# Kernel tuning notes

Hardware: AMD Instinct MI355X
Metric: run time of the kernel (lower is better)

Reference implementation:

```python
import jax, jax.numpy as jnp
import numpy as np
import math

B, S, C, H = 1, 4096, 512, 8
BLOCK = 64
NUM_RANDOM = 3


def _bigbird_mask(key):
    idx = jnp.arange(S)
    # window attention: |i - j| <= block_size // 2
    win = jnp.abs(idx[:, None] - idx[None, :]) <= (BLOCK // 2)
    # random attention: NUM_RANDOM random columns per row
    cols = jax.random.randint(key, (S, NUM_RANDOM), 0, S)
    rnd = jnp.zeros((S, S), dtype=bool).at[idx[:, None], cols].set(True)
    mask = win | rnd
    # global attention: first/last row and column attend/are attended everywhere
    mask = mask.at[0, :].set(True).at[-1, :].set(True)
    mask = mask.at[:, 0].set(True).at[:, -1].set(True)
    return mask


def setup_inputs() -> dict:
    key = jax.random.key(0)
    ks = jax.random.split(key, 7)
    xavier = lambda k: jax.random.uniform(k, (C, C), jnp.float32, -1.0, 1.0) * math.sqrt(6.0 / (C + C))
    return {
        "x": jax.random.normal(ks[0], (B, S, C), jnp.float32),
        "attn_mask": _bigbird_mask(ks[1]),
        "Wq": xavier(ks[2]), "bq": jnp.zeros((C,), jnp.float32),
        "Wk": xavier(ks[3]), "bk": jnp.zeros((C,), jnp.float32),
        "Wv": xavier(ks[4]), "bv": jnp.zeros((C,), jnp.float32),
        "Wo": xavier(ks[5]), "bo": jnp.zeros((C,), jnp.float32),
    }


def reference(x, attn_mask, Wq, bq, Wk, bk, Wv, bv, Wo, bo):
    b, s, c = x.shape
    dh = c // H
    # projections (torch Linear: x @ W.T + b)
    q = (x @ Wq.T + bq).reshape(b, s, H, dh).transpose(0, 2, 1, 3)  # [B,H,S,Dh]
    k = (x @ Wk.T + bk).reshape(b, s, H, dh).transpose(0, 2, 1, 3)
    v = (x @ Wv.T + bv).reshape(b, s, H, dh).transpose(0, 2, 1, 3)
    scores = jnp.einsum("bhsd,bhtd->bhst", q, k) / math.sqrt(dh)  # [B,H,S,S]
    scores = jnp.where(attn_mask[None, None], scores, -jnp.inf)
    attn = jax.nn.softmax(scores, axis=-1)
    out = jnp.einsum("bhst,bhtd->bhsd", attn, v)
    out = out.transpose(0, 2, 1, 3).reshape(b, s, c)
    return out @ Wo.T + bo
```

## Files before the change

### kernel.cpp

```cpp
#include <hip/hip_runtime.h>
#include <hip/hip_bf16.h>
#include <cstdint>
#include <cstddef>

#define S_LEN 4096
#define C_DIM 512
#define H_NUM 8
#define DH 64
#define MAXC 80
#define NSPLIT 64
#define DENSE_TASKS 16

typedef short short8 __attribute__((ext_vector_type(8)));
typedef float f32x4 __attribute__((ext_vector_type(4)));

__device__ __forceinline__ unsigned short f2bf(float f) {
  union { float f; uint32_t u; } c; c.f = f;
  uint32_t u = c.u;
  uint32_t r = (u + 0x7fffu + ((u >> 16) & 1u)) >> 16;
  return (unsigned short)r;
}
__device__ __forceinline__ float bf2f(unsigned short h) {
  union { uint32_t u; float f; } c; c.u = ((uint32_t)h) << 16;
  return c.f;
}

__global__ __launch_bounds__(256) void split_bf16(const float* __restrict__ src,
                                                  unsigned short* __restrict__ hi,
                                                  unsigned short* __restrict__ lo,
                                                  int n4) {
  int idx = blockIdx.x * 256 + threadIdx.x;
  if (idx >= n4) return;
  float4 v = ((const float4*)src)[idx];
  ushort4 h, l;
  h.x = f2bf(v.x); l.x = f2bf(v.x - bf2f(h.x));
  h.y = f2bf(v.y); l.y = f2bf(v.y - bf2f(h.y));
  h.z = f2bf(v.z); l.z = f2bf(v.z - bf2f(h.z));
  h.w = f2bf(v.w); l.w = f2bf(v.w - bf2f(h.w));
  ((ushort4*)hi)[idx] = h;
  ((ushort4*)lo)[idx] = l;
}

__device__ __forceinline__ void gemm_mfma_body(
    const unsigned short* __restrict__ Ah, const unsigned short* __restrict__ Al,
    const unsigned short* __restrict__ Bh, const unsigned short* __restrict__ Bl,
    const float* __restrict__ bias, float* __restrict__ C) {
  const int lane = threadIdx.x & 63;
  const int wave = threadIdx.x >> 6;
  const int m_base = blockIdx.y * 128 + (wave >> 1) * 64;
  const int n_base = blockIdx.x * 64 + (wave & 1) * 32;
  const int rfrag = lane & 15;
  const int koff = (lane >> 4) * 8;

  f32x4 acc[4][2];
#pragma unroll
  for (int mi = 0; mi < 4; ++mi)
#pragma unroll
    for (int ni = 0; ni < 2; ++ni) acc[mi][ni] = (f32x4){0.f, 0.f, 0.f, 0.f};

  for (int ks = 0; ks < C_DIM; ks += 32) {
    const int kb = ks + koff;
    short8 ah[4], al[4], bh[2], bl[2];
#pragma unroll
    for (int mi = 0; mi < 4; ++mi) {
      const size_t off = (size_t)(m_base + mi * 16 + rfrag) * C_DIM + kb;
      ah[mi] = *(const short8*)(Ah + off);
      al[mi] = *(const short8*)(Al + off);
    }
#pragma unroll
    for (int ni = 0; ni < 2; ++ni) {
      const size_t off = (size_t)(n_base + ni * 16 + rfrag) * C_DIM + kb;
      bh[ni] = *(const short8*)(Bh + off);
      bl[ni] = *(const short8*)(Bl + off);
    }
#pragma unroll
    for (int mi = 0; mi < 4; ++mi)
#pragma unroll
      for (int ni = 0; ni < 2; ++ni) {
        acc[mi][ni] = __builtin_amdgcn_mfma_f32_16x16x32_bf16(ah[mi], bh[ni], acc[mi][ni], 0, 0, 0);
        acc[mi][ni] = __builtin_amdgcn_mfma_f32_16x16x32_bf16(ah[mi], bl[ni], acc[mi][ni], 0, 0, 0);
        acc[mi][ni] = __builtin_amdgcn_mfma_f32_16x16x32_bf16(al[mi], bh[ni], acc[mi][ni], 0, 0, 0);
      }
  }

  const int col = lane & 15;
  const int r0 = (lane >> 4) * 4;
#pragma unroll
  for (int mi = 0; mi < 4; ++mi)
#pragma unroll
    for (int ni = 0; ni < 2; ++ni) {
      const float b = bias[n_base + ni * 16 + col];
#pragma unroll
      for (int r = 0; r < 4; ++r) {
        C[(size_t)(m_base + mi * 16 + r0 + r) * C_DIM + n_base + ni * 16 + col] =
            acc[mi][ni][r] + b;
      }
    }
}

__global__ __launch_bounds__(256) void qkv_gemm_mfma(
    const unsigned short* __restrict__ xh, const unsigned short* __restrict__ xl,
    const unsigned short* __restrict__ W4h, const unsigned short* __restrict__ W4l,
    const float* __restrict__ bq, const float* __restrict__ bk,
    const float* __restrict__ bv, float* __restrict__ Qbase) {
  const int z = blockIdx.z;
  const size_t NW = (size_t)C_DIM * C_DIM;
  const float* bias = (z == 0) ? bq : (z == 1) ? bk : bv;
  gemm_mfma_body(xh, xl, W4h + z * NW, W4l + z * NW, bias,
                 Qbase + z * (size_t)S_LEN * C_DIM);
}

__global__ __launch_bounds__(256) void o_gemm_mfma(
    const unsigned short* __restrict__ AOh, const unsigned short* __restrict__ AOl,
    const unsigned short* __restrict__ W4h, const unsigned short* __restrict__ W4l,
    const float* __restrict__ bo, float* __restrict__ out) {
  const size_t NW = (size_t)C_DIM * C_DIM;
  gemm_mfma_body(AOh, AOl, W4h + 3 * NW, W4l + 3 * NW, bo, out);
}

__global__ __launch_bounds__(256) void scan_mask(const uint32_t* __restrict__ mask32,
                                                 int* __restrict__ counts,
                                                 int* __restrict__ cols) {
  int i = blockIdx.x;
  int tid = threadIdx.x;
  if (i == 0 || i == S_LEN - 1) {
    if (tid == 0) counts[i] = 0;
    return;
  }
  __shared__ int cnt;
  __shared__ int list[MAXC];
  if (tid == 0) cnt = 0;
  __syncthreads();

  const bool is_b32 = (mask32[0] == 1u);
  if (is_b32) {
    const uint4* m4 = (const uint4*)(mask32 + (size_t)i * S_LEN);
#pragma unroll
    for (int q = 0; q < 4; ++q) {
      uint4 v = m4[tid * 4 + q];
      int base = tid * 16 + q * 4;
      if (v.x) { int p = atomicAdd(&cnt, 1); if (p < MAXC) list[p] = base + 0; }
      if (v.y) { int p = atomicAdd(&cnt, 1); if (p < MAXC) list[p] = base + 1; }
      if (v.z) { int p = atomicAdd(&cnt, 1); if (p < MAXC) list[p] = base + 2; }
      if (v.w) { int p = atomicAdd(&cnt, 1); if (p < MAXC) list[p] = base + 3; }
    }
  } else {
    const uint8_t* mrow = (const uint8_t*)mask32 + (size_t)i * S_LEN;
    uint4 mv = ((const uint4*)mrow)[tid];
    uint32_t w[4] = {mv.x, mv.y, mv.z, mv.w};
#pragma unroll
    for (int q = 0; q < 4; ++q)
#pragma unroll
      for (int b = 0; b < 4; ++b) {
        if ((w[q] >> (8 * b)) & 0xffu) {
          int p = atomicAdd(&cnt, 1);
          if (p < MAXC) list[p] = tid * 16 + q * 4 + b;
        }
      }
  }
  __syncthreads();
  int n = cnt < MAXC ? cnt : MAXC;
  if (tid == 0) counts[i] = n;
  for (int t = tid; t < n; t += 256) cols[(size_t)i * MAXC + t] = list[t];
}

__global__ __launch_bounds__(256) void attn_sparse(
    const float* __restrict__ Q, const float* __restrict__ K,
    const float* __restrict__ V, const int* __restrict__ counts,
    const int* __restrict__ cols, float* __restrict__ AO) {
  int wid = threadIdx.x >> 6, lane = threadIdx.x & 63;
  int task = blockIdx.x * 4 + wid;
  int i = task >> 3, h = task & 7;
  if (i == 0 || i == S_LEN - 1) return;

  __shared__ float q_lds[4][DH];
  __shared__ float ps[4][MAXC];
  __shared__ int   cs[4][MAXC];

  q_lds[wid][lane] = Q[(size_t)i * C_DIM + h * DH + lane];
  asm volatile("s_waitcnt lgkmcnt(0)" ::: "memory");
  const float4* q4 = (const float4*)q_lds[wid];

  int n = counts[i];
  if (n < 1) {
    AO[(size_t)i * C_DIM + h * DH + lane] = 0.f;
    return;
  }
  const int* cl = cols + (size_t)i * MAXC;
  int c0 = (lane < n) ? cl[lane] : 0;
  int c1 = (64 + lane < n) ? cl[64 + lane] : -1;
  bool act0 = lane < n;

  float s0 = -INFINITY, s1 = -INFINITY;
  if (act0) {
    const float4* kp = (const float4*)(K + (size_t)c0 * C_DIM + h * DH);
    float s = 0.f;
#pragma unroll
    for (int dd = 0; dd < 16; ++dd) {
      float4 kv = kp[dd], qv = q4[dd];
      s += qv.x * kv.x + qv.y * kv.y + qv.z * kv.z + qv.w * kv.w;
    }
    s0 = s * 0.125f;
  }
  if (c1 >= 0) {
    const float4* kp = (const float4*)(K + (size_t)c1 * C_DIM + h * DH);
    float s = 0.f;
#pragma unroll
    for (int dd = 0; dd < 16; ++dd) {
      float4 kv = kp[dd], qv = q4[dd];
      s += qv.x * kv.x + qv.y * kv.y + qv.z * kv.z + qv.w * kv.w;
    }
    s1 = s * 0.125f;
  }

  float mx = fmaxf(s0, s1);
#pragma unroll
  for (int off = 32; off; off >>= 1) mx = fmaxf(mx, __shfl_xor(mx, off));
  float p0 = __expf(s0 - mx);
  float p1 = __expf(s1 - mx);
  float l = p0 + p1;
#pragma unroll
  for (int off = 32; off; off >>= 1) l += __shfl_xor(l, off);
  float rl = 1.0f / l;

  ps[wid][lane] = p0 * rl;
  cs[wid][lane] = c0;
  if (lane < MAXC - 64) {
    ps[wid][64 + lane] = (c1 >= 0) ? p1 * rl : 0.f;
    cs[wid][64 + lane] = (c1 >= 0) ? c1 : 0;
  }
  asm volatile("s_waitcnt lgkmcnt(0)" ::: "memory");

  float acc = 0.f;
  const float* Vh = V + h * DH + lane;
  const int npad = (n + 7) & ~7;
  for (int j0 = 0; j0 < npad; j0 += 8) {
    float pj[8], vv[8];
#pragma unroll
    for (int u = 0; u < 8; ++u) {
      int cj = cs[wid][j0 + u];
      pj[u] = ps[wid][j0 + u];
      vv[u] = Vh[(size_t)cj * C_DIM];
    }
#pragma unroll
    for (int u = 0; u < 8; ++u) acc = fmaf(pj[u], vv[u], acc);
  }
  AO[(size_t)i * C_DIM + h * DH + lane] = acc;
}

__global__ __launch_bounds__(256) void attn_dense(const float* __restrict__ Q,
                                                  const float* __restrict__ K,
                                                  const float* __restrict__ V,
                                                  float* __restrict__ part) {
  int wid = threadIdx.x >> 6, lane = threadIdx.x & 63;
  int gid = blockIdx.x * 4 + wid;
  int task = gid >> 6;
  int split = gid & 63;
  int i = (task >> 3) ? (S_LEN - 1) : 0;
  int h = task & 7;

  __shared__ float q_lds[4][DH];
  __shared__ float pd[4][64];
  q_lds[wid][lane] = Q[(size_t)i * C_DIM + h * DH + lane];
  asm volatile("s_waitcnt lgkmcnt(0)" ::: "memory");
  const float4* q4 = (const float4*)q_lds[wid];

  const int c = split * 64 + lane;
  const float4* kp = (const float4*)(K + (size_t)c * C_DIM + h * DH);
  float s = 0.f;
#pragma unroll
  for (int dd = 0; dd < 16; ++dd) {
    float4 kv = kp[dd], qv = q4[dd];
    s += qv.x * kv.x + qv.y * kv.y + qv.z * kv.z + qv.w * kv.w;
  }
  s *= 0.125f;
  float m = s;
#pragma unroll
  for (int off = 32; off; off >>= 1) m = fmaxf(m, __shfl_xor(m, off));
  float p = __expf(s - m);
  float l = p;
#pragma unroll
  for (int off = 32; off; off >>= 1) l += __shfl_xor(l, off);

  pd[wid][lane] = p;
  asm volatile("s_waitcnt lgkmcnt(0)" ::: "memory");

  float acc = 0.f;
  const float* Vb = V + (size_t)(split * 64) * C_DIM + h * DH + lane;
  for (int j0 = 0; j0 < 64; j0 += 8) {
    float pj[8], vv[8];
#pragma unroll
    for (int u = 0; u < 8; ++u) {
      pj[u] = pd[wid][j0 + u];
      vv[u] = Vb[(size_t)(j0 + u) * C_DIM];
    }
#pragma unroll
    for (int u = 0; u < 8; ++u) acc = fmaf(pj[u], vv[u], acc);
  }
  float* pt = part + (size_t)(task * NSPLIT + split) * 68;
  pt[lane] = acc;
  if (lane == 0) {
    pt[64] = m;
    pt[65] = l;
  }
}

__global__ __launch_bounds__(64) void attn_combine(const float* __restrict__ part,
                                                   float* __restrict__ AO) {
  int task = blockIdx.x;
  int lane = threadIdx.x;
  float m = -INFINITY;
  for (int sp = 0; sp < NSPLIT; ++sp)
    m = fmaxf(m, part[(size_t)(task * NSPLIT + sp) * 68 + 64]);
  float l = 0.f, acc = 0.f;
  for (int sp = 0; sp < NSPLIT; ++sp) {
    const float* pt = part + (size_t)(task * NSPLIT + sp) * 68;
    float w = __expf(pt[64] - m);
    l += w * pt[65];
    acc += w * pt[lane];
  }
  int i = (task >> 3) ? (S_LEN - 1) : 0;
  int h = task & 7;
  AO[(size_t)i * C_DIM + h * DH + lane] = acc / l;
}

extern "C" void kernel_launch(void* const* d_in, const int* in_sizes, int n_in,
                              void* d_out, int out_size, void* d_ws,
                              size_t ws_size, hipStream_t stream) {
  const float* x = (const float*)d_in[0];
  const uint32_t* mask = (const uint32_t*)d_in[1];
  const float* Wq = (const float*)d_in[2];
  const float* bq = (const float*)d_in[3];
  const float* Wk = (const float*)d_in[4];
  const float* bk = (const float*)d_in[5];
  const float* Wv = (const float*)d_in[6];
  const float* bv = (const float*)d_in[7];
  const float* Wo = (const float*)d_in[8];
  const float* bo = (const float*)d_in[9];
  float* out = (float*)d_out;

  const size_t NELT = (size_t)S_LEN * C_DIM;
  const size_t NW = (size_t)C_DIM * C_DIM;

  float* Q = (float*)d_ws;
  float* Kb = Q + NELT;
  float* Vb = Kb + NELT;
  float* AO = Vb + NELT;
  int* counts = (int*)(AO + NELT);
  int* colsl = counts + S_LEN;
  float* part = (float*)(colsl + (size_t)S_LEN * MAXC);
  unsigned short* xh = (unsigned short*)(part + (size_t)DENSE_TASKS * NSPLIT * 68);
  unsigned short* xl = xh + NELT;
  unsigned short* AOh = xl + NELT;
  unsigned short* AOl = AOh + NELT;
  unsigned short* W4h = AOl + NELT;
  unsigned short* W4l = W4h + 4 * NW;

  scan_mask<<<S_LEN, 256, 0, stream>>>(mask, counts, colsl);

  split_bf16<<<(NELT / 4 + 255) / 256, 256, 0, stream>>>(x, xh, xl, NELT / 4);
  split_bf16<<<(NW / 4 + 255) / 256, 256, 0, stream>>>(Wq, W4h, W4l, NW / 4);
  split_bf16<<<(NW / 4 + 255) / 256, 256, 0, stream>>>(Wk, W4h + NW, W4l + NW, NW / 4);
  split_bf16<<<(NW / 4 + 255) / 256, 256, 0, stream>>>(Wv, W4h + 2 * NW, W4l + 2 * NW, NW / 4);
  split_bf16<<<(NW / 4 + 255) / 256, 256, 0, stream>>>(Wo, W4h + 3 * NW, W4l + 3 * NW, NW / 4);
  qkv_gemm_mfma<<<dim3(C_DIM / 64, S_LEN / 128, 3), 256, 0, stream>>>(
      xh, xl, W4h, W4l, bq, bk, bv, Q);

  attn_sparse<<<(S_LEN * H_NUM) / 4, 256, 0, stream>>>(Q, Kb, Vb, counts, colsl, AO);
  attn_dense<<<(DENSE_TASKS * NSPLIT) / 4, 256, 0, stream>>>(Q, Kb, Vb, part);
  attn_combine<<<DENSE_TASKS, 64, 0, stream>>>(part, AO);

  split_bf16<<<(NELT / 4 + 255) / 256, 256, 0, stream>>>(AO, AOh, AOl, NELT / 4);
  o_gemm_mfma<<<dim3(C_DIM / 64, S_LEN / 128, 1), 256, 0, stream>>>(
      AOh, AOl, W4h, W4l, bo, out);
}
```

Measured before the change: 354.8 us.

## Cooperative K-row loads in sparse attention, merge weight splits, swizzle block order

The sparse attention score step now has 16 lanes handle one column each, with 4 lanes splitting each K row into 16-float slices and reducing with shuffles. Scores go through LDS instead of each lane reading a whole 64-float K row on its own. This is meant to give coalesced K reads and avoid idle lanes when a row has fewer than 64 valid columns. Block indices are swizzled across the grid and launch bounds raised to aim for more occupancy, and the four weight-split launches become one 2D launch to save launch overhead. It adds a serial chunk loop, extra LDS traffic, and shuffle reductions.

```diff
diff --git a/kernel.cpp b/kernel.cpp
--- a/kernel.cpp
+++ b/kernel.cpp
@@ -23,6 +23,13 @@
 __device__ __forceinline__ float bf2f(unsigned short h) {
   union { uint32_t u; float f; } c; c.u = ((uint32_t)h) << 16;
   return c.f;
+}
+
+__device__ __forceinline__ void split4(float4 v, ushort4& h, ushort4& l) {
+  h.x = f2bf(v.x); l.x = f2bf(v.x - bf2f(h.x));
+  h.y = f2bf(v.y); l.y = f2bf(v.y - bf2f(h.y));
+  h.z = f2bf(v.z); l.z = f2bf(v.z - bf2f(h.z));
+  h.w = f2bf(v.w); l.w = f2bf(v.w - bf2f(h.w));
 }
 
 __global__ __launch_bounds__(256) void split_bf16(const float* __restrict__ src,
@@ -33,12 +40,24 @@
   if (idx >= n4) return;
   float4 v = ((const float4*)src)[idx];
   ushort4 h, l;
-  h.x = f2bf(v.x); l.x = f2bf(v.x - bf2f(h.x));
-  h.y = f2bf(v.y); l.y = f2bf(v.y - bf2f(h.y));
-  h.z = f2bf(v.z); l.z = f2bf(v.z - bf2f(h.z));
-  h.w = f2bf(v.w); l.w = f2bf(v.w - bf2f(h.w));
+  split4(v, h, l);
   ((ushort4*)hi)[idx] = h;
   ((ushort4*)lo)[idx] = l;
+}
+
+__global__ __launch_bounds__(256) void split_bf16_w4(
+    const float* __restrict__ Wq, const float* __restrict__ Wk,
+    const float* __restrict__ Wv, const float* __restrict__ Wo,
+    unsigned short* __restrict__ W4h, unsigned short* __restrict__ W4l) {
+  const int z = blockIdx.y;
+  const float* src = (z == 0) ? Wq : (z == 1) ? Wk : (z == 2) ? Wv : Wo;
+  const size_t NW4 = (size_t)C_DIM * C_DIM / 4;
+  int idx = blockIdx.x * 256 + threadIdx.x;
+  float4 v = ((const float4*)src)[idx];
+  ushort4 h, l;
+  split4(v, h, l);
+  ((ushort4*)(W4h))[z * NW4 + idx] = h;
+  ((ushort4*)(W4l))[z * NW4 + idx] = l;
 }
 
 __device__ __forceinline__ void gemm_mfma_body(
@@ -164,55 +183,57 @@
   for (int t = tid; t < n; t += 256) cols[(size_t)i * MAXC + t] = list[t];
 }
 
-__global__ __launch_bounds__(256) void attn_sparse(
+__global__ __launch_bounds__(256, 8) void attn_sparse(
     const float* __restrict__ Q, const float* __restrict__ K,
     const float* __restrict__ V, const int* __restrict__ counts,
     const int* __restrict__ cols, float* __restrict__ AO) {
+  int bid = blockIdx.x;
+  int bid2 = (bid & 7) * (int)(gridDim.x >> 3) + (bid >> 3);
   int wid = threadIdx.x >> 6, lane = threadIdx.x & 63;
-  int task = blockIdx.x * 4 + wid;
+  int task = bid2 * 4 + wid;
   int i = task >> 3, h = task & 7;
   if (i == 0 || i == S_LEN - 1) return;
 
   __shared__ float q_lds[4][DH];
+  __shared__ float sc[4][MAXC];
   __shared__ float ps[4][MAXC];
   __shared__ int   cs[4][MAXC];
 
+  int n = counts[i];
   q_lds[wid][lane] = Q[(size_t)i * C_DIM + h * DH + lane];
-  asm volatile("s_waitcnt lgkmcnt(0)" ::: "memory");
-  const float4* q4 = (const float4*)q_lds[wid];
-
-  int n = counts[i];
+  const int* cl = cols + (size_t)i * MAXC;
+  cs[wid][lane] = (lane < n) ? cl[lane] : 0;
+  if (lane < MAXC - 64) cs[wid][64 + lane] = (64 + lane < n) ? cl[64 + lane] : 0;
+  asm volatile("s_waitcnt lgkmcnt(0)" ::: "memory");
+
   if (n < 1) {
     AO[(size_t)i * C_DIM + h * DH + lane] = 0.f;
     return;
   }
-  const int* cl = cols + (size_t)i * MAXC;
-  int c0 = (lane < n) ? cl[lane] : 0;
-  int c1 = (64 + lane < n) ? cl[64 + lane] : -1;
-  bool act0 = lane < n;
-
-  float s0 = -INFINITY, s1 = -INFINITY;
-  if (act0) {
-    const float4* kp = (const float4*)(K + (size_t)c0 * C_DIM + h * DH);
+
+  const int qq = lane >> 4, c = lane & 15;
+  const float* qrow = q_lds[wid] + qq * 16;
+  const int nchunk = (n + 15) >> 4;
+  for (int ch = 0; ch < nchunk; ++ch) {
+    int col = cs[wid][ch * 16 + c];
+    const float4* kp = (const float4*)(K + (size_t)col * C_DIM + h * DH + qq * 16);
+    float4 kr[4];
+#pragma unroll
+    for (int dd = 0; dd < 4; ++dd) kr[dd] = kp[dd];
     float s = 0.f;
 #pragma unroll
-    for (int dd = 0; dd < 16; ++dd) {
-      float4 kv = kp[dd], qv = q4[dd];
-      s += qv.x * kv.x + qv.y * kv.y + qv.z * kv.z + qv.w * kv.w;
-    }
-    s0 = s * 0.125f;
-  }
-  if (c1 >= 0) {
-    const float4* kp = (const float4*)(K + (size_t)c1 * C_DIM + h * DH);
-    float s = 0.f;
-#pragma unroll
-    for (int dd = 0; dd < 16; ++dd) {
-      float4 kv = kp[dd], qv = q4[dd];
-      s += qv.x * kv.x + qv.y * kv.y + qv.z * kv.z + qv.w * kv.w;
-    }
-    s1 = s * 0.125f;
-  }
-
+    for (int dd = 0; dd < 4; ++dd) {
+      float4 qv = *(const float4*)(qrow + dd * 4);
+      s += kr[dd].x * qv.x + kr[dd].y * qv.y + kr[dd].z * qv.z + kr[dd].w * qv.w;
+    }
+    s += __shfl_xor(s, 16);
+    s += __shfl_xor(s, 32);
+    if (qq == 0) sc[wid][ch * 16 + c] = s * 0.125f;
+  }
+  asm volatile("s_waitcnt lgkmcnt(0)" ::: "memory");
+
+  float s0 = (lane < n) ? sc[wid][lane] : -INFINITY;
+  float s1 = (64 + lane < n) ? sc[wid][64 + lane] : -INFINITY;
   float mx = fmaxf(s0, s1);
 #pragma unroll
   for (int off = 32; off; off >>= 1) mx = fmaxf(mx, __shfl_xor(mx, off));
@@ -224,11 +245,7 @@
   float rl = 1.0f / l;
 
   ps[wid][lane] = p0 * rl;
-  cs[wid][lane] = c0;
-  if (lane < MAXC - 64) {
-    ps[wid][64 + lane] = (c1 >= 0) ? p1 * rl : 0.f;
-    cs[wid][64 + lane] = (c1 >= 0) ? c1 : 0;
-  }
+  if (lane < MAXC - 64) ps[wid][64 + lane] = p1 * rl;
   asm volatile("s_waitcnt lgkmcnt(0)" ::: "memory");
 
   float acc = 0.f;
@@ -238,9 +255,8 @@
     float pj[8], vv[8];
 #pragma unroll
     for (int u = 0; u < 8; ++u) {
-      int cj = cs[wid][j0 + u];
       pj[u] = ps[wid][j0 + u];
-      vv[u] = Vh[(size_t)cj * C_DIM];
+      vv[u] = Vh[(size_t)cs[wid][j0 + u] * C_DIM];
     }
 #pragma unroll
     for (int u = 0; u < 8; ++u) acc = fmaf(pj[u], vv[u], acc);
@@ -359,10 +375,7 @@
   scan_mask<<<S_LEN, 256, 0, stream>>>(mask, counts, colsl);
 
   split_bf16<<<(NELT / 4 + 255) / 256, 256, 0, stream>>>(x, xh, xl, NELT / 4);
-  split_bf16<<<(NW / 4 + 255) / 256, 256, 0, stream>>>(Wq, W4h, W4l, NW / 4);
-  split_bf16<<<(NW / 4 + 255) / 256, 256, 0, stream>>>(Wk, W4h + NW, W4l + NW, NW / 4);
-  split_bf16<<<(NW / 4 + 255) / 256, 256, 0, stream>>>(Wv, W4h + 2 * NW, W4l + 2 * NW, NW / 4);
-  split_bf16<<<(NW / 4 + 255) / 256, 256, 0, stream>>>(Wo, W4h + 3 * NW, W4l + 3 * NW, NW / 4);
+  split_bf16_w4<<<dim3(NW / 4 / 256, 4), 256, 0, stream>>>(Wq, Wk, Wv, Wo, W4h, W4l);
   qkv_gemm_mfma<<<dim3(C_DIM / 64, S_LEN / 128, 3), 256, 0, stream>>>(
       xh, xl, W4h, W4l, bq, bk, bv, Q);
 
```

Measured after the change: 336.5 us. 5.2% less time.
